# Kernel tuning notes

Hardware: AMD Instinct MI355X
Metric: run time of the kernel (lower is better)

## Reference

```python
import jax, jax.numpy as jnp
import numpy as np

WIN = 4096   # win_size == nfft
HOP = 2048   # hop_size == win_size // 2 (COLA)


def _hann_periodic(n):
    # torch.hann_window default is periodic
    return (0.5 * (1.0 - jnp.cos(2.0 * jnp.pi * jnp.arange(n) / n))).astype(jnp.float32)


def _stft(x):
    # x: [B, L] real. Pad to multiple of HOP (as in get_stft_torch), then
    # frame with center=False, apply periodic Hann, one-sided rfft.
    L = x.shape[-1]
    pad = (-L) % HOP
    x = jnp.pad(x, ((0, 0), (0, pad)))
    Lp = L + pad
    T = 1 + (Lp - WIN) // HOP  # number of frames, static
    idx = jnp.arange(T)[:, None] * HOP + jnp.arange(WIN)[None, :]
    frames = x[:, idx] * _hann_periodic(WIN)
    S = jnp.fft.rfft(frames, axis=-1)
    return jnp.swapaxes(S, -1, -2)  # [B, F, T]


def _edr_db(S):
    # Energy decay relief: suffix sum of |S|^2 over time, in dB.
    # Replaces the original O(T^2) per-frame loop with a reverse cumsum.
    p = (S.real * S.real + S.imag * S.imag).astype(jnp.float32)  # [B, F, T]
    suffix = jnp.cumsum(p[..., ::-1], axis=-1)[..., ::-1]
    return 10.0 * jnp.log10(suffix)  # db(x, is_squared=True)


def setup_inputs() -> dict:
    key = jax.random.key(0)
    k1, k2 = jax.random.split(key)
    B, NFREQ = 32, 192000
    return {
        "target_response": jax.random.normal(k1, (B, NFREQ), dtype=jnp.float32),
        "achieved_response": jax.random.normal(k2, (B, NFREQ), dtype=jnp.float32),
    }


def reference(target_response, achieved_response):
    n = target_response.shape[-1]
    # torch.fft.irfft(x, n=x.shape[-1]) -> time-domain RIR of length n
    target_rir = jnp.fft.irfft(target_response, n=n).astype(jnp.float32)
    achieved_rir = jnp.fft.irfft(achieved_response, n=n).astype(jnp.float32)

    S_target = _stft(target_rir)   # [B, F, T] complex64
    S_ach = _stft(achieved_rir)

    target_edr = _edr_db(S_target)  # [B, F, T] float32
    ach_edr = _edr_db(S_ach)

    freq_loss = jnp.sum(jnp.abs(target_edr - ach_edr), axis=-1)  # [B, F]
    loss_per_item = jnp.sum(freq_loss, axis=-1) / jnp.sum(
        jnp.abs(target_edr), axis=(-2, -1)
    )  # [B]
    return jnp.sum(loss_per_item)
```

## Files before the change

kernel.cpp:

```cpp
#include <hip/hip_runtime.h>
#include <hip/hip_fp16.h>
#include <math.h>

#define NSIG 64
#define NROW 192000
#define NN   192000
#define LP   192512
#define NT   93
#define NF   2049
#define PSTR 2050
#define PTS  (NT*PSTR)
#define NK2  188
#define TWO_PI 6.28318530717958647692f
#define SQ2H  0.70710678118654752440f
#define DB_LOG2 3.01029995663981195f

#define WS_P_OFF   0
#define WS_A_OFF   24403200ULL
#define WS_Y_OFF   49044736ULL
#define WS_ACC_OFF 73686272ULL

__device__ __forceinline__ float2 cmul(float2 a, float2 b) {
    return make_float2(a.x*b.x - a.y*b.y, a.x*b.y + a.y*b.x);
}
__device__ __forceinline__ float2 cadd(float2 a, float2 b) {
    return make_float2(a.x + b.x, a.y + b.y);
}
__device__ __forceinline__ float2 csub(float2 a, float2 b) {
    return make_float2(a.x - b.x, a.y - b.y);
}
__device__ __forceinline__ float2 mul_nI(float2 z) { return make_float2(z.y, -z.x); }
__device__ __forceinline__ float2 mul_pI(float2 z) { return make_float2(-z.y, z.x); }
__device__ __forceinline__ __half2 f2h(float2 v) { return __float22half2_rn(v); }
__device__ __forceinline__ float2 h2f(__half2 h) { return __half22float2(h); }

__device__ __forceinline__ void dft8(float2 (&x)[8]) {
    float2 e0 = cadd(x[0], x[4]), e1 = csub(x[0], x[4]);
    float2 e2 = cadd(x[2], x[6]), e3 = csub(x[2], x[6]);
    float2 E0 = cadd(e0, e2), E2 = csub(e0, e2);
    float2 E1 = cadd(e1, mul_nI(e3)), E3 = csub(e1, mul_nI(e3));
    float2 o0 = cadd(x[1], x[5]), o1 = csub(x[1], x[5]);
    float2 o2 = cadd(x[3], x[7]), o3 = csub(x[3], x[7]);
    float2 O0 = cadd(o0, o2), O2 = csub(o0, o2);
    float2 O1 = cadd(o1, mul_nI(o3)), O3 = csub(o1, mul_nI(o3));
    float2 W1 = make_float2(SQ2H*(O1.x + O1.y), SQ2H*(O1.y - O1.x));
    float2 W2 = mul_nI(O2);
    float2 W3 = make_float2(SQ2H*(O3.y - O3.x), -SQ2H*(O3.x + O3.y));
    x[0] = cadd(E0, O0); x[4] = csub(E0, O0);
    x[1] = cadd(E1, W1); x[5] = csub(E1, W1);
    x[2] = cadd(E2, W2); x[6] = csub(E2, W2);
    x[3] = cadd(E3, W3); x[7] = csub(E3, W3);
}

__device__ __forceinline__ void dft8i(float2 (&x)[8]) {
    float2 e0 = cadd(x[0], x[4]), e1 = csub(x[0], x[4]);
    float2 e2 = cadd(x[2], x[6]), e3 = csub(x[2], x[6]);
    float2 E0 = cadd(e0, e2), E2 = csub(e0, e2);
    float2 E1 = cadd(e1, mul_pI(e3)), E3 = csub(e1, mul_pI(e3));
    float2 o0 = cadd(x[1], x[5]), o1 = csub(x[1], x[5]);
    float2 o2 = cadd(x[3], x[7]), o3 = csub(x[3], x[7]);
    float2 O0 = cadd(o0, o2), O2 = csub(o0, o2);
    float2 O1 = cadd(o1, mul_pI(o3)), O3 = csub(o1, mul_pI(o3));
    float2 W1 = make_float2(SQ2H*(O1.x - O1.y), SQ2H*(O1.x + O1.y));
    float2 W2 = mul_pI(O2);
    float2 W3 = make_float2(-SQ2H*(O3.x + O3.y), SQ2H*(O3.x - O3.y));
    x[0] = cadd(E0, O0); x[4] = csub(E0, O0);
    x[1] = cadd(E1, W1); x[5] = csub(E1, W1);
    x[2] = cadd(E2, W2); x[6] = csub(E2, W2);
    x[3] = cadd(E3, W3); x[7] = csub(E3, W3);
}

#define S3C 0.86602540378443865f
__device__ __forceinline__ void dft3i(float2& x0, float2& x1, float2& x2) {
    float2 u = cadd(x1, x2), v = csub(x1, x2);
    float2 w = make_float2(x0.x - 0.5f*u.x, x0.y - 0.5f*u.y);
    x0 = cadd(x0, u);
    float2 iv = make_float2(-S3C * v.y, S3C * v.x);
    x1 = cadd(w, iv);
    x2 = csub(w, iv);
}

#define C51 0.30901699437494742f
#define S51 0.95105651629515357f
#define C52 (-0.80901699437494742f)
#define S52 0.58778525229247313f
__device__ __forceinline__ void dft5i(float2& x0, float2& x1, float2& x2,
                                      float2& x3, float2& x4) {
    float2 t1 = cadd(x1, x4), t2 = csub(x1, x4);
    float2 t3 = cadd(x2, x3), t4 = csub(x2, x3);
    float2 s0 = x0;
    x0 = make_float2(s0.x + t1.x + t3.x, s0.y + t1.y + t3.y);
    float2 A1 = make_float2(s0.x + C51*t1.x + C52*t3.x, s0.y + C51*t1.y + C52*t3.y);
    float2 B1 = make_float2(S51*t2.x + S52*t4.x, S51*t2.y + S52*t4.y);
    float2 A2 = make_float2(s0.x + C52*t1.x + C51*t3.x, s0.y + C52*t1.y + C51*t3.y);
    float2 B2 = make_float2(S52*t2.x - S51*t4.x, S52*t2.y - S51*t4.y);
    x1 = make_float2(A1.x - B1.y, A1.y + B1.x);
    x4 = make_float2(A1.x + B1.y, A1.y - B1.x);
    x2 = make_float2(A2.x - B2.y, A2.y + B2.x);
    x3 = make_float2(A2.x + B2.y, A2.y - B2.x);
}

#define SSTR 520
__global__ void __launch_bounds__(256) k_stage1(const float* __restrict__ X0,
                                                const float* __restrict__ X1,
                                                __half2* __restrict__ A) {
    const int bid  = blockIdx.x;
    const int sig  = bid & 63;
    const int kb   = bid >> 6;
    const int base = kb * 16;
    const float* X = (sig < 32) ? (X0 + (size_t)sig * NROW)
                                : (X1 + (size_t)(sig - 32) * NROW);
    __shared__ float SR[8 * SSTR], SI[8 * SSTR];
    const int tid = threadIdx.x;
    const int row = tid & 7;
    const int ln  = tid >> 3;

    const int k2e0 = base + 2 * row;
    const int k2e  = (k2e0 < NK2) ? k2e0 : (NK2 - 1);
    const int k2o  = (k2e0 + 1 < NK2) ? (k2e0 + 1) : (NK2 - 1);

    #pragma unroll
    for (int m = 0; m < 16; ++m) {
        int i = ln + 32 * m;
        int ide = 375 * i + k2e;
        int ido = 375 * i + k2o;
        float xe = X[(ide <= 96000) ? ide : (NN - ide)];
        float xo = X[(ido <= 96000) ? ido : (NN - ido)];
        SR[SSTR * row + i] = xe;
        SI[SSTR * row + i] = xo;
    }
    __syncthreads();

    const int w = tid >> 6;
    const int l = tid & 63;
    float* sra = SR + SSTR * (2 * w);     float* sia = SI + SSTR * (2 * w);
    float* srb = SR + SSTR * (2 * w + 1); float* sib = SI + SSTR * (2 * w + 1);
    float2 xa[8], xb[8];

    #pragma unroll
    for (int n1 = 0; n1 < 8; ++n1) {
        int ad = l + 64 * n1;
        xa[n1] = make_float2(sra[ad], sia[ad]);
        xb[n1] = make_float2(srb[ad], sib[ad]);
    }
    dft8i(xa); dft8i(xb);
    {
        float sn, cs; __sincosf(TWO_PI * (float)l * (1.0f / 512.0f), &sn, &cs);
        float2 bw = make_float2(cs, sn), tw = bw;
        xa[1] = cmul(xa[1], tw); xb[1] = cmul(xb[1], tw);
        #pragma unroll
        for (int k = 2; k < 8; ++k) {
            tw = cmul(tw, bw);
            xa[k] = cmul(xa[k], tw); xb[k] = cmul(xb[k], tw);
        }
    }
    #pragma unroll
    for (int a2 = 0; a2 < 8; ++a2) {
        int ad = 64 * a2 + (l ^ (8 * a2));
        sra[ad] = xa[a2].x; sia[ad] = xa[a2].y;
        srb[ad] = xb[a2].x; sib[ad] = xb[a2].y;
    }
    __builtin_amdgcn_wave_barrier();

    const int l0 = l & 7, aa = l >> 3;
    #pragma unroll
    for (int l1 = 0; l1 < 8; ++l1) {
        int ad = 64 * aa + ((l0 + 8 * l1) ^ (8 * aa));
        xa[l1] = make_float2(sra[ad], sia[ad]);
        xb[l1] = make_float2(srb[ad], sib[ad]);
    }
    dft8i(xa); dft8i(xb);
    {
        float sn, cs; __sincosf(TWO_PI * (float)l0 * (1.0f / 64.0f), &sn, &cs);
        float2 bw = make_float2(cs, sn), tw = bw;
        xa[1] = cmul(xa[1], tw); xb[1] = cmul(xb[1], tw);
        #pragma unroll
        for (int k = 2; k < 8; ++k) {
            tw = cmul(tw, bw);
            xa[k] = cmul(xa[k], tw); xb[k] = cmul(xb[k], tw);
        }
    }
    #pragma unroll
    for (int b2 = 0; b2 < 8; ++b2) {
        int ad = 64 * b2 + 8 * aa + (l0 ^ b2);
        sra[ad] = xa[b2].x; sia[ad] = xa[b2].y;
        srb[ad] = xb[b2].x; sib[ad] = xb[b2].y;
    }
    __builtin_amdgcn_wave_barrier();

    const int a3 = l & 7, b3 = l >> 3;
    #pragma unroll
    for (int l0r = 0; l0r < 8; ++l0r) {
        int ad = 64 * b3 + 8 * a3 + (l0r ^ b3);
        xa[l0r] = make_float2(sra[ad], sia[ad]);
        xb[l0r] = make_float2(srb[ad], sib[ad]);
    }
    dft8i(xa); dft8i(xb);
    #pragma unroll
    for (int c = 0; c < 8; ++c) {
        int ad = a3 + 8 * b3 + 64 * c;
        sra[ad] = xa[c].x; sia[ad] = xa[c].y;
        srb[ad] = xb[c].x; sib[ad] = xb[c].y;
    }
    __syncthreads();

    if (k2e0 < NK2) {
        float sn, cs;
        __sincosf(TWO_PI * (float)(k2e * ln) * (1.0f / 192000.0f), &sn, &cs);
        float2 wke = make_float2(cs, sn);
        __sincosf(TWO_PI * (float)(32 * k2e) * (1.0f / 192000.0f), &sn, &cs);
        float2 ste = make_float2(cs, sn);
        __sincosf(TWO_PI * (float)(k2o * ln) * (1.0f / 192000.0f), &sn, &cs);
        float2 wko = make_float2(cs, sn);
        __sincosf(TWO_PI * (float)(32 * k2o) * (1.0f / 192000.0f), &sn, &cs);
        float2 sto = make_float2(cs, sn);
        const bool odd_ok = (k2e0 + 1 < NK2);
        __half2* Ae = A + ((size_t)sig * NK2 + k2e) * 512;
        __half2* Ao = A + ((size_t)sig * NK2 + k2o) * 512;
        const float* zr = SR + SSTR * row;
        const float* zi = SI + SSTR * row;
        #pragma unroll
        for (int m = 0; m < 16; ++m) {
            int k  = ln + 32 * m;
            int km = (512 - k) & 511;
            float2 Z  = make_float2(zr[k],  zi[k]);
            float2 Zm = make_float2(zr[km], zi[km]);
            float2 S = make_float2(Z.x + Zm.x, Z.y - Zm.y);
            float2 D = make_float2(Z.x - Zm.x, Z.y + Zm.y);
            float2 Xe = make_float2(0.5f * S.x, 0.5f * S.y);
            float2 Xo = make_float2(0.5f * D.y, -0.5f * D.x);
            Ae[k] = f2h(cmul(Xe, wke));
            if (odd_ok) Ao[k] = f2h(cmul(Xo, wko));
            wke = cmul(wke, ste);
            wko = cmul(wko, sto);
        }
    }
}

#define TT2 16
#define T1STR 17
__global__ void __launch_bounds__(256) k_stage2(const __half2* __restrict__ A,
                                                __half* __restrict__ Y) {
    const int t1b = blockIdx.x * TT2;
    const int sig = blockIdx.y;
    __shared__ float SRT[375 * T1STR], SIT[375 * T1STR];
    const int tid = threadIdx.x;

    if (blockIdx.x == 0) {
        for (int j = tid; j < 512; j += 256)
            Y[(size_t)sig * LP + NN + j] = __float2half(0.f);
    }

    for (int w = tid; w < 25 * TT2; w += 256) {
        int c = w >> 4, t1l = w & 15;
        float2 v[15];
        const __half2* As = A + (size_t)sig * (NK2 * 512) + t1b + t1l;
        #pragma unroll
        for (int a = 0; a < 15; ++a) {
            int k2 = 25 * a + c;
            if (k2 < NK2) {
                v[a] = h2f(As[(size_t)k2 * 512]);
            } else {
                float2 u = h2f(As[(size_t)(375 - k2) * 512]);
                v[a] = make_float2(u.x, -u.y);
            }
        }
        #pragma unroll
        for (int r = 0; r < 5; ++r) dft3i(v[r], v[r + 5], v[r + 10]);
        float2 tw[15];
        tw[0] = make_float2(1.f, 0.f);
        float sn, cs; __sincosf(TWO_PI * (float)c * (1.0f / 375.0f), &sn, &cs);
        float2 stp = make_float2(cs, sn);
        #pragma unroll
        for (int e = 1; e < 15; ++e) tw[e] = cmul(tw[e - 1], stp);
        #pragma unroll
        for (int e3 = 0; e3 < 3; ++e3) {
            float2 h0 = v[5 * e3], h1, h2, h3, h4;
            if (e3 == 0) { h1 = v[1]; h2 = v[2]; h3 = v[3]; h4 = v[4]; }
            else if (e3 == 1) {
                h1 = cmul(v[6],  make_float2(0.91354545764260090f, 0.40673664307580021f));
                h2 = cmul(v[7],  make_float2(0.66913060635885821f, 0.74314482547739424f));
                h3 = cmul(v[8],  make_float2(0.30901699437494742f, 0.95105651629515357f));
                h4 = cmul(v[9],  make_float2(-0.10452846326765347f, 0.99452189536827334f));
            } else {
                h1 = cmul(v[11], make_float2(0.66913060635885821f, 0.74314482547739424f));
                h2 = cmul(v[12], make_float2(-0.10452846326765347f, 0.99452189536827334f));
                h3 = cmul(v[13], make_float2(-0.80901699437494742f, 0.58778525229247313f));
                h4 = cmul(v[14], make_float2(-0.97814760073380564f, -0.20791169081775934f));
            }
            dft5i(h0, h1, h2, h3, h4);
            float2 o0 = cmul(h0, tw[e3]);
            float2 o1 = cmul(h1, tw[e3 + 3]);
            float2 o2 = cmul(h2, tw[e3 + 6]);
            float2 o3 = cmul(h3, tw[e3 + 9]);
            float2 o4 = cmul(h4, tw[e3 + 12]);
            int r0 = ((e3     ) * 25 + c) * T1STR + t1l;
            int r1 = ((e3 + 3 ) * 25 + c) * T1STR + t1l;
            int r2 = ((e3 + 6 ) * 25 + c) * T1STR + t1l;
            int r3 = ((e3 + 9 ) * 25 + c) * T1STR + t1l;
            int r4 = ((e3 + 12) * 25 + c) * T1STR + t1l;
            SRT[r0] = o0.x; SIT[r0] = o0.y;
            SRT[r1] = o1.x; SIT[r1] = o1.y;
            SRT[r2] = o2.x; SIT[r2] = o2.y;
            SRT[r3] = o3.x; SIT[r3] = o3.y;
            SRT[r4] = o4.x; SIT[r4] = o4.y;
        }
    }
    __syncthreads();

    if (tid < 15 * TT2) {
        int e = tid >> 4, t1l = tid & 15;
        float2 t[25];
        #pragma unroll
        for (int c = 0; c < 25; ++c) {
            int rr = (e * 25 + c) * T1STR + t1l;
            t[c] = make_float2(SRT[rr], SIT[rr]);
        }
        #pragma unroll
        for (int c2 = 0; c2 < 5; ++c2)
            dft5i(t[c2], t[c2 + 5], t[c2 + 10], t[c2 + 15], t[c2 + 20]);
        t[6]  = cmul(t[6],  make_float2(0.96858316112863108f, 0.24868988716485479f));
        t[11] = cmul(t[11], make_float2(0.87630668004386358f, 0.48175367410171532f));
        t[16] = cmul(t[16], make_float2(0.72896862742141155f, 0.68454710592868873f));
        t[21] = cmul(t[21], make_float2(0.53582679497899666f, 0.84432792550201508f));
        t[7]  = cmul(t[7],  make_float2(0.87630668004386358f, 0.48175367410171532f));
        t[12] = cmul(t[12], make_float2(0.53582679497899666f, 0.84432792550201508f));
        t[17] = cmul(t[17], make_float2(0.06279051952931337f, 0.99802672842827156f));
        t[22] = cmul(t[22], make_float2(-0.42577929156507272f, 0.90482705246601958f));
        t[8]  = cmul(t[8],  make_float2(0.72896862742141155f, 0.68454710592868873f));
        t[13] = cmul(t[13], make_float2(0.06279051952931337f, 0.99802672842827156f));
        t[18] = cmul(t[18], make_float2(-0.63742398974868975f, 0.77051324277578925f));
        t[23] = cmul(t[23], make_float2(-0.99211470131447788f, 0.12533323356430426f));
        t[9]  = cmul(t[9],  make_float2(0.53582679497899666f, 0.84432792550201508f));
        t[14] = cmul(t[14], make_float2(-0.42577929156507272f, 0.90482705246601958f));
        t[19] = cmul(t[19], make_float2(-0.99211470131447788f, 0.12533323356430426f));
        t[24] = cmul(t[24], make_float2(-0.63742398974868997f, -0.77051324277578903f));
        #pragma unroll
        for (int u5 = 0; u5 < 5; ++u5)
            dft5i(t[5*u5], t[5*u5 + 1], t[5*u5 + 2], t[5*u5 + 3], t[5*u5 + 4]);
        __half* yb = Y + (size_t)sig * LP + t1b + t1l;
        #pragma unroll
        for (int u5 = 0; u5 < 5; ++u5)
            #pragma unroll
            for (int u5p = 0; u5p < 5; ++u5p) {
                int d = u5 + 5 * u5p;
                yb[(size_t)(512 * (15 * d + e))] =
                    __float2half_rn(t[5 * u5 + u5p].x * (1.0f / 192000.0f));
            }
    }
}

__global__ void __launch_bounds__(256) k_stft(const __half* __restrict__ Y,
                                              __half* __restrict__ P,
                                              float* __restrict__ ACC) {
    const int bid = blockIdx.x;
    const int sig = bid & 63;
    const int fr  = bid >> 6;
    const int lt  = threadIdx.x;
    __shared__ float SR[2560], SI[2560];
    __shared__ float2 wt2[32];
    float2 x[8];
    float2 base2048;

    if (bid == 0 && lt < 64) ACC[lt] = 0.f;

    {
        const __half2* yb = (const __half2*)(Y + (size_t)sig * LP + (size_t)fr * 2048);
        float sn, cs;
        __sincosf(TWO_PI * (float)lt * (1.0f / 2048.0f), &sn, &cs);
        base2048 = make_float2(cs, sn);
        float2 ce = base2048;
        const float2 d1 = make_float2(0.99999882345170188f,
                                      0.00153398018628477f);
        float2 co = cmul(ce, d1);
        const float2 r45 = make_float2(SQ2H, SQ2H);
        #pragma unroll
        for (int r = 0; r < 8; ++r) {
            float2 v = h2f(yb[lt + 256 * r]);
            float we = 0.5f - 0.5f * ce.x;
            float wo = 0.5f - 0.5f * co.x;
            x[r] = make_float2(v.x * we, v.y * wo);
            ce = cmul(ce, r45);
            co = cmul(co, r45);
        }
    }
    dft8(x);
    {
        float2 b = make_float2(base2048.x, -base2048.y), tw = b;
        x[1] = cmul(x[1], tw);
        #pragma unroll
        for (int k = 2; k < 8; ++k) { tw = cmul(tw, b); x[k] = cmul(x[k], tw); }
    }
    #pragma unroll
    for (int k = 0; k < 8; ++k) { SR[k * 256 + lt] = x[k].x; SI[k * 256 + lt] = x[k].y; }
    if (lt < 32) {
        float sn, cs; __sincosf(-TWO_PI * (float)lt * (1.0f / 256.0f), &sn, &cs);
        wt2[lt] = make_float2(cs, sn);
    }
    __syncthreads();

    {
        const int k2 = lt >> 5, m1 = lt & 31;
        #pragma unroll
        for (int r = 0; r < 8; ++r) {
            int idx = k2 * 256 + m1 + 32 * r;
            x[r] = make_float2(SR[idx], SI[idx]);
        }
        dft8(x);
        float2 b = wt2[m1], tw = b;
        x[1] = cmul(x[1], tw);
        #pragma unroll
        for (int k = 2; k < 8; ++k) { tw = cmul(tw, b); x[k] = cmul(x[k], tw); }
        __syncthreads();
        #pragma unroll
        for (int j = 0; j < 8; ++j) {
            int idx = k2 * 288 + j * 36 + m1;
            SR[idx] = x[j].x; SI[idx] = x[j].y;
        }
    }
    __syncthreads();

    {
        const int k2 = lt >> 5, j2 = (lt >> 2) & 7, p1 = lt & 3;
        #pragma unroll
        for (int r = 0; r < 8; ++r) {
            int idx = k2 * 288 + j2 * 36 + p1 + 4 * r;
            x[r] = make_float2(SR[idx], SI[idx]);
        }
        dft8(x);
        float2 b = (p1 == 0) ? make_float2(1.f, 0.f)
                 : (p1 == 1) ? make_float2(0.98078528040323044f, -0.19509032201612827f)
                 : (p1 == 2) ? make_float2(0.92387953251128676f, -0.38268343236508977f)
                 :             make_float2(0.83146961230254524f, -0.55557023301960222f);
        float2 tw = b;
        x[1] = cmul(x[1], tw);
        #pragma unroll
        for (int k = 2; k < 8; ++k) { tw = cmul(tw, b); x[k] = cmul(x[k], tw); }
        __syncthreads();
        #pragma unroll
        for (int q = 0; q < 8; ++q) {
            int idx = 5 * (q * 64 + k2 * 8 + j2) + p1;
            SR[idx] = x[q].x; SI[idx] = x[q].y;
        }
    }
    __syncthreads();

    {
        float2 za[4], zb[4];
        #pragma unroll
        for (int p = 0; p < 4; ++p) {
            int ia = 5 * lt + p;
            za[p] = make_float2(SR[ia], SI[ia]);
            zb[p] = make_float2(SR[ia + 1280], SI[ia + 1280]);
        }
        __syncthreads();
        const int q2a = lt >> 6, k2 = (lt >> 3) & 7, j2 = lt & 7;
        const int kbase = k2 + 8 * j2;
        {
            float2 s0 = cadd(za[0], za[2]), s1 = csub(za[0], za[2]);
            float2 s2 = cadd(za[1], za[3]), s3 = csub(za[1], za[3]);
            float2 X0 = cadd(s0, s2), X2 = csub(s0, s2);
            float2 X1 = cadd(s1, mul_nI(s3)), X3 = csub(s1, mul_nI(s3));
            int ka = kbase + 64 * q2a;
            SR[ka]        = X0.x; SI[ka]        = X0.y;
            SR[ka + 512]  = X1.x; SI[ka + 512]  = X1.y;
            SR[ka + 1024] = X2.x; SI[ka + 1024] = X2.y;
            SR[ka + 1536] = X3.x; SI[ka + 1536] = X3.y;
        }
        {
            float2 s0 = cadd(zb[0], zb[2]), s1 = csub(zb[0], zb[2]);
            float2 s2 = cadd(zb[1], zb[3]), s3 = csub(zb[1], zb[3]);
            float2 X0 = cadd(s0, s2), X2 = csub(s0, s2);
            float2 X1 = cadd(s1, mul_nI(s3)), X3 = csub(s1, mul_nI(s3));
            int kb = kbase + 64 * (q2a + 4);
            SR[kb]        = X0.x; SI[kb]        = X0.y;
            SR[kb + 512]  = X1.x; SI[kb + 512]  = X1.y;
            SR[kb + 1024] = X2.x; SI[kb + 1024] = X2.y;
            SR[kb + 1536] = X3.x; SI[kb + 1536] = X3.y;
        }
    }
    __syncthreads();

    {
        __half* pb = P + (size_t)sig * PTS + (size_t)fr * PSTR;
        float c2 = sqrtf(0.5f * (1.f + base2048.x));
        float s2 = sqrtf(0.5f * (1.f - base2048.x));
        float2 wk = make_float2(c2, -s2);
        const float2 stp = make_float2(0.92387953251128676f,
                                       -0.38268343236508977f);
        #pragma unroll
        for (int j = 0; j < 8; ++j) {
            int k  = lt + 256 * j;
            int kc = (2048 - k) & 2047;
            float zr = SR[k],  zi = SI[k];
            float cr = SR[kc], ci = SI[kc];
            float Ex = 0.5f * (zr + cr), Ey = 0.5f * (zi - ci);
            float Ox = 0.5f * (zi + ci), Oy = -0.5f * (zr - cr);
            float Xx = Ex + wk.x * Ox - wk.y * Oy;
            float Xy = Ey + wk.x * Oy + wk.y * Ox;
            pb[k] = __float2half_rn(sqrtf(Xx * Xx + Xy * Xy));
            wk = cmul(wk, stp);
        }
        if (lt == 0) { float d0 = SR[0] - SI[0]; pb[2048] = __float2half_rn(fabsf(d0)); }
    }
}

__global__ void __launch_bounds__(256) k_edr(const __half* __restrict__ P,
                                             float* __restrict__ ACC) {
    const int b = blockIdx.y;
    const int f = blockIdx.x * 256 + threadIdx.x;
    const bool act = (f < NF);
    const __half* Pt = P + (size_t)b * PTS;
    const __half* Pa = P + (size_t)(b + 32) * PTS;
    float st = 0.f, sa = 0.f, num = 0.f, den = 0.f;
    if (act) {
        for (int t = NT - 1; t >= 0; --t) {
            float vt = __half2float(Pt[(size_t)t * PSTR + f]);
            float va = __half2float(Pa[(size_t)t * PSTR + f]);
            st += vt * vt;
            sa += va * va;
            float et = DB_LOG2 * __log2f(st);
            float ea = DB_LOG2 * __log2f(sa);
            num += fabsf(et - ea);
            den += fabsf(et);
        }
    }
    for (int off = 32; off > 0; off >>= 1) {
        num += __shfl_down(num, off);
        den += __shfl_down(den, off);
    }
    __shared__ float sn_[4], sd_[4];
    int wave = threadIdx.x >> 6, lane = threadIdx.x & 63;
    if (lane == 0) { sn_[wave] = num; sd_[wave] = den; }
    __syncthreads();
    if (threadIdx.x == 0) {
        float n = sn_[0] + sn_[1] + sn_[2] + sn_[3];
        float d = sd_[0] + sd_[1] + sd_[2] + sd_[3];
        atomicAdd(&ACC[2 * b], n);
        atomicAdd(&ACC[2 * b + 1], d);
    }
}

__global__ void k_final(const float* __restrict__ ACC, float* __restrict__ out) {
    int tid = threadIdx.x;
    float r = 0.f;
    if (tid < 32) r = ACC[2 * tid] / ACC[2 * tid + 1];
    for (int off = 32; off > 0; off >>= 1) r += __shfl_down(r, off);
    if (tid == 0) out[0] = r;
}

extern "C" void kernel_launch(void* const* d_in, const int* in_sizes, int n_in,
                              void* d_out, int out_size, void* d_ws, size_t ws_size,
                              hipStream_t stream) {
    const float* X0 = (const float*)d_in[0];
    const float* X1 = (const float*)d_in[1];
    float* out = (float*)d_out;

    char* base = (char*)d_ws;
    __half*  P  = (__half*)(base + WS_P_OFF);
    __half2* A  = (__half2*)(base + WS_A_OFF);
    __half*  Y  = (__half*)(base + WS_Y_OFF);
    float*   ACC = (float*)(base + WS_ACC_OFF);

    k_stage1<<<dim3(768),      dim3(256), 0, stream>>>(X0, X1, A);
    k_stage2<<<dim3(32, 64),   dim3(256), 0, stream>>>(A, Y);
    k_stft  <<<dim3(5952),     dim3(256), 0, stream>>>(Y, P, ACC);
    k_edr   <<<dim3(9, 32),    dim3(256), 0, stream>>>(P, ACC);
    k_final <<<1, 64, 0, stream>>>(ACC, out);
}
```

Baseline: 88.29 us.

## Pack two real column transforms into one complex FFT in stage2

Stage2 now processes two adjacent t1 columns per thread by combining them as a + i*b into a single complex 375-point DFT. The real output goes in the real part and the second column's output in the imaginary part, written as a half2 pair. This halves the FFT arithmetic and the grid size, and replaces scalar half loads and stores with wider packed accesses. It relies on the inverse transform outputs being real, which holds because the stage1 data is Hermitian.

```diff
diff --git a/kernel.cpp b/kernel.cpp
--- a/kernel.cpp
+++ b/kernel.cpp
@@ -237,11 +237,11 @@
     }
 }
 
-#define TT2 16
+#define TP2 16
 #define T1STR 17
 __global__ void __launch_bounds__(256) k_stage2(const __half2* __restrict__ A,
                                                 __half* __restrict__ Y) {
-    const int t1b = blockIdx.x * TT2;
+    const int t1b = blockIdx.x * (2 * TP2);
     const int sig = blockIdx.y;
     __shared__ float SRT[375 * T1STR], SIT[375 * T1STR];
     const int tid = threadIdx.x;
@@ -251,18 +251,23 @@
             Y[(size_t)sig * LP + NN + j] = __float2half(0.f);
     }
 
-    for (int w = tid; w < 25 * TT2; w += 256) {
-        int c = w >> 4, t1l = w & 15;
+    for (int w = tid; w < 25 * TP2; w += 256) {
+        int c = w >> 4, pl = w & 15;
         float2 v[15];
-        const __half2* As = A + (size_t)sig * (NK2 * 512) + t1b + t1l;
+        const float2* Asf = (const float2*)(A + (size_t)sig * (NK2 * 512) + t1b + 2 * pl);
         #pragma unroll
         for (int a = 0; a < 15; ++a) {
             int k2 = 25 * a + c;
             if (k2 < NK2) {
-                v[a] = h2f(As[(size_t)k2 * 512]);
+                float2 raw = Asf[(size_t)k2 * 256];
+                float2 fa = h2f(((const __half2*)&raw)[0]);
+                float2 fb = h2f(((const __half2*)&raw)[1]);
+                v[a] = make_float2(fa.x - fb.y, fa.y + fb.x);
             } else {
-                float2 u = h2f(As[(size_t)(375 - k2) * 512]);
-                v[a] = make_float2(u.x, -u.y);
+                float2 raw = Asf[(size_t)(375 - k2) * 256];
+                float2 fa = h2f(((const __half2*)&raw)[0]);
+                float2 fb = h2f(((const __half2*)&raw)[1]);
+                v[a] = make_float2(fa.x + fb.y, fb.x - fa.y);
             }
         }
         #pragma unroll
@@ -294,11 +299,11 @@
             float2 o2 = cmul(h2, tw[e3 + 6]);
             float2 o3 = cmul(h3, tw[e3 + 9]);
             float2 o4 = cmul(h4, tw[e3 + 12]);
-            int r0 = ((e3     ) * 25 + c) * T1STR + t1l;
-            int r1 = ((e3 + 3 ) * 25 + c) * T1STR + t1l;
-            int r2 = ((e3 + 6 ) * 25 + c) * T1STR + t1l;
-            int r3 = ((e3 + 9 ) * 25 + c) * T1STR + t1l;
-            int r4 = ((e3 + 12) * 25 + c) * T1STR + t1l;
+            int r0 = ((e3     ) * 25 + c) * T1STR + pl;
+            int r1 = ((e3 + 3 ) * 25 + c) * T1STR + pl;
+            int r2 = ((e3 + 6 ) * 25 + c) * T1STR + pl;
+            int r3 = ((e3 + 9 ) * 25 + c) * T1STR + pl;
+            int r4 = ((e3 + 12) * 25 + c) * T1STR + pl;
             SRT[r0] = o0.x; SIT[r0] = o0.y;
             SRT[r1] = o1.x; SIT[r1] = o1.y;
             SRT[r2] = o2.x; SIT[r2] = o2.y;
@@ -308,12 +313,12 @@
     }
     __syncthreads();
 
-    if (tid < 15 * TT2) {
-        int e = tid >> 4, t1l = tid & 15;
+    if (tid < 15 * TP2) {
+        int e = tid >> 4, pl = tid & 15;
         float2 t[25];
         #pragma unroll
         for (int c = 0; c < 25; ++c) {
-            int rr = (e * 25 + c) * T1STR + t1l;
+            int rr = (e * 25 + c) * T1STR + pl;
             t[c] = make_float2(SRT[rr], SIT[rr]);
         }
         #pragma unroll
@@ -338,14 +343,16 @@
         #pragma unroll
         for (int u5 = 0; u5 < 5; ++u5)
             dft5i(t[5*u5], t[5*u5 + 1], t[5*u5 + 2], t[5*u5 + 3], t[5*u5 + 4]);
-        __half* yb = Y + (size_t)sig * LP + t1b + t1l;
+        __half2* yb2 = (__half2*)(Y + (size_t)sig * LP + t1b + 2 * pl);
         #pragma unroll
         for (int u5 = 0; u5 < 5; ++u5)
             #pragma unroll
             for (int u5p = 0; u5p < 5; ++u5p) {
                 int d = u5 + 5 * u5p;
-                yb[(size_t)(512 * (15 * d + e))] =
-                    __float2half_rn(t[5 * u5 + u5p].x * (1.0f / 192000.0f));
+                float2 wv = t[5 * u5 + u5p];
+                yb2[(size_t)256 * (15 * d + e)] =
+                    __floats2half2_rn(wv.x * (1.0f / 192000.0f),
+                                      wv.y * (1.0f / 192000.0f));
             }
     }
 }
@@ -563,7 +570,7 @@
     float*   ACC = (float*)(base + WS_ACC_OFF);
 
     k_stage1<<<dim3(768),      dim3(256), 0, stream>>>(X0, X1, A);
-    k_stage2<<<dim3(32, 64),   dim3(256), 0, stream>>>(A, Y);
+    k_stage2<<<dim3(16, 64),   dim3(256), 0, stream>>>(A, Y);
     k_stft  <<<dim3(5952),     dim3(256), 0, stream>>>(Y, P, ACC);
     k_edr   <<<dim3(9, 32),    dim3(256), 0, stream>>>(P, ACC);
     k_final <<<1, 64, 0, stream>>>(ACC, out);
```

New measurement: 79.20 us (median of 3 runs). 10.3% less time.
